# Kernel tuning notes

Measured on AMD Instinct MI355X. Metric: run time of the kernel, lower is better.

Reference implementation:

```python
import jax, jax.numpy as jnp
import numpy as np

N_NODES = 100000
N_EDGES = 1_600_000
N_ROIS = 400
HIDDEN = 128
N_GRAPHS = 512
OUT = 2


def setup_inputs() -> dict:
    key = jax.random.key(0)
    ks = jax.random.split(key, 7)
    x = jax.random.normal(ks[0], (N_NODES, N_ROIS), dtype=jnp.float32)
    edge_index = jax.random.randint(ks[1], (2, N_EDGES), 0, N_NODES, dtype=jnp.int32)
    # sorted graph-assignment vector; prepend arange so every graph id is non-empty
    rnd = jax.random.randint(ks[2], (N_NODES - N_GRAPHS,), 0, N_GRAPHS, dtype=jnp.int32)
    batch = jnp.sort(jnp.concatenate([jnp.arange(N_GRAPHS, dtype=jnp.int32), rnd]))
    W = jax.random.normal(ks[3], (N_ROIS, HIDDEN), dtype=jnp.float32) / np.float32(np.sqrt(N_ROIS))
    b = jnp.zeros((HIDDEN,), dtype=jnp.float32)
    lin_W = jax.random.normal(ks[4], (HIDDEN, OUT), dtype=jnp.float32) / np.float32(np.sqrt(HIDDEN))
    lin_b = jnp.zeros((OUT,), dtype=jnp.float32)
    return {"x": x, "edge_index": edge_index, "batch": batch,
            "W": W, "b": b, "lin_W": lin_W, "lin_b": lin_b}


def reference(x, edge_index, batch, W, b, lin_W, lin_b):
    N = x.shape[0]
    # GCNConv: add self-loops, symmetric normalization D^-1/2 (A+I) D^-1/2
    loops = jnp.arange(N, dtype=edge_index.dtype)
    row = jnp.concatenate([edge_index[0], loops])  # source
    col = jnp.concatenate([edge_index[1], loops])  # target
    deg = jax.ops.segment_sum(jnp.ones_like(col, dtype=x.dtype), col, num_segments=N)
    dinv = jnp.where(deg > 0, jax.lax.rsqrt(deg), 0.0)
    norm = dinv[row] * dinv[col]                   # [E+N]
    h = x @ W                                      # [N, H] transform before propagate
    msg = h[row] * norm[:, None]                   # [E+N, H]
    agg = jax.ops.segment_sum(msg, col, num_segments=N) + b
    act = jax.nn.relu(agg)                         # [N, H]
    # global max pool over graph ids (all segments guaranteed non-empty)
    pooled = jax.ops.segment_max(act, batch, num_segments=N_GRAPHS)  # [G, H]
    logits = pooled @ lin_W + lin_b                # [G, OUT]
    return logits, pooled
```

## Files before the change

kernel.cpp:

```cpp
#include <hip/hip_runtime.h>
#include <hip/hip_bf16.h>

#define N_NODES 100000
#define N_EDGES 1600000
#define N_ROIS  400
#define HID     128
#define N_GRAPHS 512
#define NOUT    2
#define NBUCK   391
#define BCAP    8192
#define ECH     4096
#define NPW     16
#define NBLK_BUCKET 391
#define NBLK_PREP   208
#define NBLK_GEMM   782

typedef __attribute__((ext_vector_type(8))) short short8;
typedef __attribute__((ext_vector_type(4))) float f32x4;

static __device__ __forceinline__ unsigned short f2bf(float f) {
  unsigned u = __float_as_uint(f);
  u += 0x7fffu + ((u >> 16) & 1u);
  return (unsigned short)(u >> 16);
}
static __device__ __forceinline__ float bf2f(unsigned short h) {
  return __uint_as_float(((unsigned)h) << 16);
}

static __device__ __forceinline__ void gload_lds16(const unsigned short* g, short* l) {
  __builtin_amdgcn_global_load_lds(
      (const __attribute__((address_space(1))) void*)g,
      (__attribute__((address_space(3))) void*)l, 16, 0, 0);
}

__global__ __launch_bounds__(256) void prep_bucket_k(
    const int* __restrict__ row, const int* __restrict__ col,
    int* __restrict__ bcnt, unsigned int* __restrict__ pairs,
    const float* __restrict__ W, unsigned short* __restrict__ Wf) {
  __shared__ int hist[NBUCK];
  __shared__ int base[NBUCK];
  int t = threadIdx.x;
  if (blockIdx.x >= NBLK_BUCKET) {
    int idx = (blockIdx.x - NBLK_BUCKET) * 256 + t;
    if (idx < 13 * 8 * 64 * 8) {
      int u    = idx & 7;
      int lane = (idx >> 3) & 63;
      int nt   = (idx >> 9) & 7;
      int kk5  = idx >> 12;
      int n = nt * 16 + (lane & 15);
      int k = kk5 * 32 + (lane >> 4) * 8 + u;
      Wf[idx] = (k < N_ROIS) ? f2bf(W[k * HID + n]) : (unsigned short)0;
    }
    return;
  }
  for (int b = t; b < NBUCK; b += 256) hist[b] = 0;
  __syncthreads();
  int e0 = blockIdx.x * ECH;
  unsigned int pk[16];
  int bk[16], rk[16];
#pragma unroll
  for (int i = 0; i < 16; ++i) {
    int e = e0 + t + i * 256;
    if (e < N_EDGES) {
      int r = row[e], c = col[e];
      bk[i] = c >> 8;
      pk[i] = ((unsigned)r << 8) | (unsigned)(c & 255);
      rk[i] = atomicAdd(&hist[bk[i]], 1);
    } else bk[i] = -1;
  }
  __syncthreads();
  for (int b = t; b < NBUCK; b += 256)
    base[b] = (hist[b] > 0) ? atomicAdd(&bcnt[b], hist[b]) : 0;
  __syncthreads();
#pragma unroll
  for (int i = 0; i < 16; ++i)
    if (bk[i] >= 0) {
      int p = base[bk[i]] + rk[i];
      if (p < BCAP) pairs[(size_t)bk[i] * BCAP + p] = pk[i];
    }
}

__global__ __launch_bounds__(512, 4) void csr_gemm_k(
    const unsigned int* __restrict__ pairs, const int* __restrict__ bcnt,
    int* __restrict__ csr_row, int* __restrict__ offs, int* __restrict__ cnt,
    float* __restrict__ dinv,
    const float* __restrict__ x, const unsigned short* __restrict__ Wf,
    unsigned short* __restrict__ hp) {
  __shared__ __align__(16) union {
    struct { unsigned int ep[BCAP]; int h[256]; int sc[256]; int cur[256]; } c;
    short Bs[28672];
  } u;
  int t = threadIdx.x;

  if (blockIdx.x < NBUCK) {
    bool act = t < 256;
    int b = blockIdx.x;
    int m = min(bcnt[b], BCAP);
    size_t base = (size_t)b * BCAP;
    for (int j = t; j < m; j += 512) u.c.ep[j] = pairs[base + j];
    if (act) u.c.h[t] = 0;
    __syncthreads();
    for (int j = t; j < m; j += 512) atomicAdd(&u.c.h[u.c.ep[j] & 255u], 1);
    __syncthreads();
    int myc = act ? u.c.h[t] : 0;
    int mycp = (myc + 3) & ~3;
    if (act) u.c.sc[t] = mycp;
    __syncthreads();
    for (int off = 1; off < 256; off <<= 1) {
      int v = (act && t >= off) ? u.c.sc[t - off] : 0;
      __syncthreads();
      if (act) u.c.sc[t] += v;
      __syncthreads();
    }
    if (act) {
      int loff = u.c.sc[t] - mycp;
      u.c.cur[t] = loff;
      int node = b * 256 + t;
      if (node < N_NODES) {
        cnt[node] = myc;
        offs[node] = (int)base + loff;
        dinv[node] = rsqrtf((float)(myc + 1));
      }
    }
    __syncthreads();
    for (int j = t; j < m; j += 512) {
      unsigned int e = u.c.ep[j];
      int pos = atomicAdd(&u.c.cur[e & 255u], 1);
      if (pos < BCAP) csr_row[base + pos] = (int)(e >> 8);
    }
    return;
  }

  int lane = t & 63, wv = t >> 6;
  int mrow = lane & 15, kg = lane >> 4;
  int row0 = (blockIdx.x - NBUCK) * 128;
  int arow = row0 + wv * 16 + mrow;
  bool rowok = arow < N_NODES;
  const float* xp = x + (size_t)arow * N_ROIS;

  f32x4 acc[8];
#pragma unroll
  for (int i = 0; i < 8; ++i) acc[i] = (f32x4){0.f, 0.f, 0.f, 0.f};

#pragma unroll
  for (int c = 0; c < 7; ++c) {
    int ch = wv * 7 + c;
    gload_lds16(Wf + (size_t)ch * 512 + lane * 8, &u.Bs[ch * 512]);
  }
  asm volatile("s_waitcnt vmcnt(0)" ::: "memory");
  __syncthreads();

#pragma unroll
  for (int kf = 0; kf < 7; ++kf) {
    int k0 = kf * 32 + kg * 8;
    short8 a8;
    if (rowok && k0 + 8 <= N_ROIS) {
      float4 f0 = *(const float4*)(xp + k0);
      float4 f1 = *(const float4*)(xp + k0 + 4);
      a8[0] = (short)f2bf(f0.x); a8[1] = (short)f2bf(f0.y);
      a8[2] = (short)f2bf(f0.z); a8[3] = (short)f2bf(f0.w);
      a8[4] = (short)f2bf(f1.x); a8[5] = (short)f2bf(f1.y);
      a8[6] = (short)f2bf(f1.z); a8[7] = (short)f2bf(f1.w);
    } else {
#pragma unroll
      for (int v = 0; v < 8; ++v) {
        int k = k0 + v;
        float f = (rowok && k < N_ROIS) ? xp[k] : 0.f;
        a8[v] = (short)f2bf(f);
      }
    }
#pragma unroll
    for (int nt = 0; nt < 8; ++nt) {
      short8 bf = *(const short8*)&u.Bs[(kf * 8 + nt) * 512 + lane * 8];
      acc[nt] = __builtin_amdgcn_mfma_f32_16x16x32_bf16(a8, bf, acc[nt], 0, 0, 0);
    }
  }
  __syncthreads();

#pragma unroll
  for (int c = 0; c < 6; ++c) {
    int ch = wv * 6 + c;
    gload_lds16(Wf + (size_t)(56 + ch) * 512 + lane * 8, &u.Bs[ch * 512]);
  }
  asm volatile("s_waitcnt vmcnt(0)" ::: "memory");
  __syncthreads();

#pragma unroll
  for (int kf = 0; kf < 6; ++kf) {
    int k0 = (kf + 7) * 32 + kg * 8;
    short8 a8;
    if (rowok && k0 + 8 <= N_ROIS) {
      float4 f0 = *(const float4*)(xp + k0);
      float4 f1 = *(const float4*)(xp + k0 + 4);
      a8[0] = (short)f2bf(f0.x); a8[1] = (short)f2bf(f0.y);
      a8[2] = (short)f2bf(f0.z); a8[3] = (short)f2bf(f0.w);
      a8[4] = (short)f2bf(f1.x); a8[5] = (short)f2bf(f1.y);
      a8[6] = (short)f2bf(f1.z); a8[7] = (short)f2bf(f1.w);
    } else {
#pragma unroll
      for (int v = 0; v < 8; ++v) {
        int k = k0 + v;
        float f = (rowok && k < N_ROIS) ? xp[k] : 0.f;
        a8[v] = (short)f2bf(f);
      }
    }
#pragma unroll
    for (int nt = 0; nt < 8; ++nt) {
      short8 bf = *(const short8*)&u.Bs[(kf * 8 + nt) * 512 + lane * 8];
      acc[nt] = __builtin_amdgcn_mfma_f32_16x16x32_bf16(a8, bf, acc[nt], 0, 0, 0);
    }
  }

#pragma unroll
  for (int r = 0; r < 4; ++r) {
    int grow = row0 + wv * 16 + kg * 4 + r;
    if (grow < N_NODES) {
      unsigned short* op = hp + (size_t)grow * HID + mrow;
#pragma unroll
      for (int nt = 0; nt < 8; ++nt) op[nt * 16] = f2bf(acc[nt][r]);
    }
  }
}

static __device__ __forceinline__ void acc8s(float* a, uint4 u, float d) {
  a[0] = fmaf(d, bf2f((unsigned short)(u.x)), a[0]);
  a[1] = fmaf(d, bf2f((unsigned short)(u.x >> 16)), a[1]);
  a[2] = fmaf(d, bf2f((unsigned short)(u.y)), a[2]);
  a[3] = fmaf(d, bf2f((unsigned short)(u.y >> 16)), a[3]);
  a[4] = fmaf(d, bf2f((unsigned short)(u.z)), a[4]);
  a[5] = fmaf(d, bf2f((unsigned short)(u.z >> 16)), a[5]);
  a[6] = fmaf(d, bf2f((unsigned short)(u.w)), a[6]);
  a[7] = fmaf(d, bf2f((unsigned short)(u.w >> 16)), a[7]);
}

__global__ __launch_bounds__(256) void gather_k(
    const unsigned short* __restrict__ hp, const int* __restrict__ csr_row,
    const int* __restrict__ offs, const int* __restrict__ cnt,
    const float* __restrict__ dinv, const int* __restrict__ batch,
    const float* __restrict__ bias, unsigned int* __restrict__ pooled_bits) {
  int wave = (blockIdx.x * blockDim.x + threadIdx.x) >> 6;
  int lane = threadIdx.x & 63;
  int g  = lane >> 4;
  int cg = lane & 15;
  int n0 = wave * NPW;
  if (n0 >= N_NODES) return;
  int nend = min(n0 + NPW, N_NODES);
  float bv[8];
  {
    float4 b0 = *(const float4*)(bias + cg * 8);
    float4 b1 = *(const float4*)(bias + cg * 8 + 4);
    bv[0] = b0.x; bv[1] = b0.y; bv[2] = b0.z; bv[3] = b0.w;
    bv[4] = b1.x; bv[5] = b1.y; bv[6] = b1.z; bv[7] = b1.w;
  }
  float rm[8];
#pragma unroll
  for (int k = 0; k < 8; ++k) rm[k] = 0.f;
  int cur_g = batch[n0];

  for (int i = n0; i < nend; ++i) {
    int start = offs[i];
    int m = cnt[i];
    float di = dinv[i];
    float a[8];
#pragma unroll
    for (int k = 0; k < 8; ++k) a[k] = 0.f;
    if (g == 0) {
      uint4 u = *(const uint4*)(hp + (size_t)i * HID + cg * 8);
      acc8s(a, u, di);
    }
    for (int j = 0; j < m; j += 4) {
      int4 q = *(const int4*)(csr_row + start + j);
      int s = (g == 0) ? q.x : (g == 1) ? q.y : (g == 2) ? q.z : q.w;
      if (j + g < m) {
        float dv = dinv[s];
        uint4 u = *(const uint4*)(hp + (size_t)s * HID + cg * 8);
        acc8s(a, u, dv);
      }
    }
#pragma unroll
    for (int k = 0; k < 8; ++k) {
      a[k] += __shfl_xor(a[k], 16);
      a[k] += __shfl_xor(a[k], 32);
    }
    int gb = batch[i];
    if (gb != cur_g) {
      if (lane < 16) {
#pragma unroll
        for (int k = 0; k < 8; ++k)
          atomicMax(&pooled_bits[cur_g * HID + cg * 8 + k], __float_as_uint(rm[k]));
      }
#pragma unroll
      for (int k = 0; k < 8; ++k) rm[k] = 0.f;
      cur_g = gb;
    }
#pragma unroll
    for (int k = 0; k < 8; ++k)
      rm[k] = fmaxf(rm[k], fmaxf(fmaf(di, a[k], bv[k]), 0.f));
  }
  if (lane < 16) {
#pragma unroll
    for (int k = 0; k < 8; ++k)
      atomicMax(&pooled_bits[cur_g * HID + cg * 8 + k], __float_as_uint(rm[k]));
  }
}

__global__ void logits_k(const float* __restrict__ pooled, const float* __restrict__ lin_W,
                         const float* __restrict__ lin_b, float* __restrict__ out) {
  int t = blockIdx.x * blockDim.x + threadIdx.x;
  if (t < N_GRAPHS * NOUT) {
    int g = t >> 1, o = t & 1;
    float s = lin_b[o];
    const float* pg = pooled + g * HID;
#pragma unroll 8
    for (int k = 0; k < HID; ++k) s = fmaf(pg[k], lin_W[k * NOUT + o], s);
    out[t] = s;
  }
}

extern "C" void kernel_launch(void* const* d_in, const int* in_sizes, int n_in,
                              void* d_out, int out_size, void* d_ws, size_t ws_size,
                              hipStream_t stream) {
  (void)in_sizes; (void)n_in; (void)ws_size;
  const float* x     = (const float*)d_in[0];
  const int*   ei    = (const int*)d_in[1];
  const int*   row   = ei;
  const int*   col   = ei + N_EDGES;
  const int*   batch = (const int*)d_in[2];
  const float* W     = (const float*)d_in[3];
  const float* b     = (const float*)d_in[4];
  const float* lin_W = (const float*)d_in[5];
  const float* lin_b = (const float*)d_in[6];
  float* out = (float*)d_out;

  char* ws = (char*)d_ws;
  int*   bcnt    = (int*)(ws + 0);
  int*   offs    = (int*)(ws + 4096);
  int*   cnt     = (int*)(ws + 404096);
  float* dinv    = (float*)(ws + 804096);
  unsigned short* Wf = (unsigned short*)(ws + 1204096);
  int*   csr_row = (int*)(ws + 1310720);
  unsigned int* pairs = (unsigned int*)(ws + 14123008);
  unsigned short* hp  = (unsigned short*)(ws + 26935296);

  hipMemsetAsync(bcnt, 0, NBUCK * sizeof(int), stream);
  hipMemsetAsync(d_out, 0, (size_t)out_size * sizeof(float), stream);

  prep_bucket_k<<<NBLK_BUCKET + NBLK_PREP, 256, 0, stream>>>(row, col, bcnt, pairs, W, Wf);
  csr_gemm_k<<<NBUCK + NBLK_GEMM, 512, 0, stream>>>(
      pairs, bcnt, csr_row, offs, cnt, dinv, x, Wf, hp);
  {
    int waves = (N_NODES + NPW - 1) / NPW;
    int blocks = (waves * 64 + 255) / 256;
    gather_k<<<blocks, 256, 0, stream>>>(
        hp, csr_row, offs, cnt, dinv, batch, b,
        (unsigned int*)(out + N_GRAPHS * NOUT));
  }
  logits_k<<<(N_GRAPHS * NOUT + 255) / 256, 256, 0, stream>>>(
      out + N_GRAPHS * NOUT, lin_W, lin_b, out);
}
```

Before: 385.5 us.

## Split hidden features into eight column slabs for cache-local gather

Measured after the change: 633.4 us. 1.64x slower.

```diff
diff --git a/kernel.cpp b/kernel.cpp
--- a/kernel.cpp
+++ b/kernel.cpp
@@ -14,6 +14,7 @@
 #define NBLK_BUCKET 391
 #define NBLK_PREP   208
 #define NBLK_GEMM   782
+#define SLAB ((size_t)N_NODES * 16)
 
 typedef __attribute__((ext_vector_type(8))) short short8;
 typedef __attribute__((ext_vector_type(4))) float f32x4;
@@ -85,7 +86,7 @@
     int* __restrict__ csr_row, int* __restrict__ offs, int* __restrict__ cnt,
     float* __restrict__ dinv,
     const float* __restrict__ x, const unsigned short* __restrict__ Wf,
-    unsigned short* __restrict__ hp) {
+    unsigned short* __restrict__ hp2) {
   __shared__ __align__(16) union {
     struct { unsigned int ep[BCAP]; int h[256]; int sc[256]; int cur[256]; } c;
     short Bs[28672];
@@ -215,9 +216,9 @@
   for (int r = 0; r < 4; ++r) {
     int grow = row0 + wv * 16 + kg * 4 + r;
     if (grow < N_NODES) {
-      unsigned short* op = hp + (size_t)grow * HID + mrow;
-#pragma unroll
-      for (int nt = 0; nt < 8; ++nt) op[nt * 16] = f2bf(acc[nt][r]);
+#pragma unroll
+      for (int nt = 0; nt < 8; ++nt)
+        hp2[(size_t)nt * SLAB + (size_t)grow * 16 + mrow] = f2bf(acc[nt][r]);
     }
   }
 }
@@ -234,21 +235,24 @@
 }
 
 __global__ __launch_bounds__(256) void gather_k(
-    const unsigned short* __restrict__ hp, const int* __restrict__ csr_row,
+    const unsigned short* __restrict__ hp2, const int* __restrict__ csr_row,
     const int* __restrict__ offs, const int* __restrict__ cnt,
     const float* __restrict__ dinv, const int* __restrict__ batch,
     const float* __restrict__ bias, unsigned int* __restrict__ pooled_bits) {
-  int wave = (blockIdx.x * blockDim.x + threadIdx.x) >> 6;
+  int slice = blockIdx.x & 7;
+  int bslot = blockIdx.x >> 3;
   int lane = threadIdx.x & 63;
-  int g  = lane >> 4;
-  int cg = lane & 15;
-  int n0 = wave * NPW;
+  int wv = threadIdx.x >> 6;
+  int n0 = (bslot * 4 + wv) * NPW;
   if (n0 >= N_NODES) return;
   int nend = min(n0 + NPW, N_NODES);
+  int es = lane >> 1;
+  int ch = lane & 1;
+  const unsigned short* hs = hp2 + (size_t)slice * SLAB;
   float bv[8];
   {
-    float4 b0 = *(const float4*)(bias + cg * 8);
-    float4 b1 = *(const float4*)(bias + cg * 8 + 4);
+    float4 b0 = *(const float4*)(bias + slice * 16 + ch * 8);
+    float4 b1 = *(const float4*)(bias + slice * 16 + ch * 8 + 4);
     bv[0] = b0.x; bv[1] = b0.y; bv[2] = b0.z; bv[3] = b0.w;
     bv[4] = b1.x; bv[5] = b1.y; bv[6] = b1.z; bv[7] = b1.w;
   }
@@ -264,30 +268,34 @@
     float a[8];
 #pragma unroll
     for (int k = 0; k < 8; ++k) a[k] = 0.f;
-    if (g == 0) {
-      uint4 u = *(const uint4*)(hp + (size_t)i * HID + cg * 8);
+    if (es == 0) {
+      uint4 u = *(const uint4*)(hs + (size_t)i * 16 + ch * 8);
       acc8s(a, u, di);
     }
-    for (int j = 0; j < m; j += 4) {
-      int4 q = *(const int4*)(csr_row + start + j);
-      int s = (g == 0) ? q.x : (g == 1) ? q.y : (g == 2) ? q.z : q.w;
-      if (j + g < m) {
+    for (int j = 0; j < m; j += 32) {
+      int idx = j + es;
+      if (idx < m) {
+        int s = csr_row[start + idx];
         float dv = dinv[s];
-        uint4 u = *(const uint4*)(hp + (size_t)s * HID + cg * 8);
+        uint4 u = *(const uint4*)(hs + (size_t)s * 16 + ch * 8);
         acc8s(a, u, dv);
       }
     }
 #pragma unroll
     for (int k = 0; k < 8; ++k) {
+      a[k] += __shfl_xor(a[k], 2);
+      a[k] += __shfl_xor(a[k], 4);
+      a[k] += __shfl_xor(a[k], 8);
       a[k] += __shfl_xor(a[k], 16);
       a[k] += __shfl_xor(a[k], 32);
     }
     int gb = batch[i];
     if (gb != cur_g) {
-      if (lane < 16) {
+      if (lane < 2) {
 #pragma unroll
         for (int k = 0; k < 8; ++k)
-          atomicMax(&pooled_bits[cur_g * HID + cg * 8 + k], __float_as_uint(rm[k]));
+          atomicMax(&pooled_bits[cur_g * HID + slice * 16 + ch * 8 + k],
+                    __float_as_uint(rm[k]));
       }
 #pragma unroll
       for (int k = 0; k < 8; ++k) rm[k] = 0.f;
@@ -297,10 +305,11 @@
     for (int k = 0; k < 8; ++k)
       rm[k] = fmaxf(rm[k], fmaxf(fmaf(di, a[k], bv[k]), 0.f));
   }
-  if (lane < 16) {
+  if (lane < 2) {
 #pragma unroll
     for (int k = 0; k < 8; ++k)
-      atomicMax(&pooled_bits[cur_g * HID + cg * 8 + k], __float_as_uint(rm[k]));
+      atomicMax(&pooled_bits[cur_g * HID + slice * 16 + ch * 8 + k],
+                __float_as_uint(rm[k]));
   }
 }
 
@@ -340,19 +349,19 @@
   unsigned short* Wf = (unsigned short*)(ws + 1204096);
   int*   csr_row = (int*)(ws + 1310720);
   unsigned int* pairs = (unsigned int*)(ws + 14123008);
-  unsigned short* hp  = (unsigned short*)(ws + 26935296);
+  unsigned short* hp2 = (unsigned short*)(ws + 26935296);
 
   hipMemsetAsync(bcnt, 0, NBUCK * sizeof(int), stream);
   hipMemsetAsync(d_out, 0, (size_t)out_size * sizeof(float), stream);
 
   prep_bucket_k<<<NBLK_BUCKET + NBLK_PREP, 256, 0, stream>>>(row, col, bcnt, pairs, W, Wf);
   csr_gemm_k<<<NBUCK + NBLK_GEMM, 512, 0, stream>>>(
-      pairs, bcnt, csr_row, offs, cnt, dinv, x, Wf, hp);
+      pairs, bcnt, csr_row, offs, cnt, dinv, x, Wf, hp2);
   {
-    int waves = (N_NODES + NPW - 1) / NPW;
-    int blocks = (waves * 64 + 255) / 256;
-    gather_k<<<blocks, 256, 0, stream>>>(
-        hp, csr_row, offs, cnt, dinv, batch, b,
+    int waves_per_slice = (N_NODES + NPW - 1) / NPW;
+    int blocks_per_slice = (waves_per_slice + 3) / 4;
+    gather_k<<<8 * blocks_per_slice, 256, 0, stream>>>(
+        hp2, csr_row, offs, cnt, dinv, batch, b,
         (unsigned int*)(out + N_GRAPHS * NOUT));
   }
   logits_k<<<(N_GRAPHS * NOUT + 255) / 256, 256, 0, stream>>>(
```

## Stage bucket scatters in LDS to coalesce global writes of pairs and CSR rows

Applied to the files above, without the earlier changes.

Result: no change. 381.7 us (-1.0%).

```diff
diff --git a/kernel.cpp b/kernel.cpp
--- a/kernel.cpp
+++ b/kernel.cpp
@@ -38,7 +38,11 @@
     int* __restrict__ bcnt, unsigned int* __restrict__ pairs,
     const float* __restrict__ W, unsigned short* __restrict__ Wf) {
   __shared__ int hist[NBUCK];
-  __shared__ int base[NBUCK];
+  __shared__ int lbase[NBUCK];
+  __shared__ int adj[NBUCK];
+  __shared__ unsigned int spk[ECH];
+  __shared__ unsigned short sbk[ECH];
+  __shared__ int sc[256];
   int t = threadIdx.x;
   if (blockIdx.x >= NBLK_BUCKET) {
     int idx = (blockIdx.x - NBLK_BUCKET) * 256 + t;
@@ -56,6 +60,7 @@
   for (int b = t; b < NBUCK; b += 256) hist[b] = 0;
   __syncthreads();
   int e0 = blockIdx.x * ECH;
+  int mtot = min(ECH, N_EDGES - e0);
   unsigned int pk[16];
   int bk[16], rk[16];
 #pragma unroll
@@ -69,15 +74,44 @@
     } else bk[i] = -1;
   }
   __syncthreads();
-  for (int b = t; b < NBUCK; b += 256)
-    base[b] = (hist[b] > 0) ? atomicAdd(&bcnt[b], hist[b]) : 0;
+  int v0 = hist[t];
+  sc[t] = v0;
+  __syncthreads();
+  for (int off = 1; off < 256; off <<= 1) {
+    int v = (t >= off) ? sc[t - off] : 0;
+    __syncthreads();
+    sc[t] += v;
+    __syncthreads();
+  }
+  lbase[t] = sc[t] - v0;
+  int tot0 = sc[255];
+  __syncthreads();
+  int v1 = (t < NBUCK - 256) ? hist[256 + t] : 0;
+  sc[t] = v1;
+  __syncthreads();
+  for (int off = 1; off < 256; off <<= 1) {
+    int v = (t >= off) ? sc[t - off] : 0;
+    __syncthreads();
+    sc[t] += v;
+    __syncthreads();
+  }
+  if (t < NBUCK - 256) lbase[256 + t] = tot0 + sc[t] - v1;
   __syncthreads();
 #pragma unroll
   for (int i = 0; i < 16; ++i)
     if (bk[i] >= 0) {
-      int p = base[bk[i]] + rk[i];
-      if (p < BCAP) pairs[(size_t)bk[i] * BCAP + p] = pk[i];
-    }
+      int pos = lbase[bk[i]] + rk[i];
+      spk[pos] = pk[i];
+      sbk[pos] = (unsigned short)bk[i];
+    }
+  for (int b = t; b < NBUCK; b += 256)
+    adj[b] = (hist[b] > 0) ? atomicAdd(&bcnt[b], hist[b]) : 0;
+  __syncthreads();
+  for (int j = t; j < mtot; j += 256) {
+    int b = sbk[j];
+    int p = adj[b] + (j - lbase[b]);
+    if (p < BCAP) pairs[(size_t)b * BCAP + p] = spk[j];
+  }
 }
 
 __global__ __launch_bounds__(512, 4) void csr_gemm_k(
@@ -87,7 +121,11 @@
     const float* __restrict__ x, const unsigned short* __restrict__ Wf,
     unsigned short* __restrict__ hp) {
   __shared__ __align__(16) union {
-    struct { unsigned int ep[BCAP]; int h[256]; int sc[256]; int cur[256]; } c;
+    struct {
+      unsigned int ep[BCAP];
+      int ssr[BCAP];
+      int h[256]; int sc2[256]; int cur[256];
+    } c;
     short Bs[28672];
   } u;
   int t = threadIdx.x;
@@ -104,16 +142,16 @@
     __syncthreads();
     int myc = act ? u.c.h[t] : 0;
     int mycp = (myc + 3) & ~3;
-    if (act) u.c.sc[t] = mycp;
+    if (act) u.c.sc2[t] = mycp;
     __syncthreads();
     for (int off = 1; off < 256; off <<= 1) {
-      int v = (act && t >= off) ? u.c.sc[t - off] : 0;
+      int v = (act && t >= off) ? u.c.sc2[t - off] : 0;
       __syncthreads();
-      if (act) u.c.sc[t] += v;
+      if (act) u.c.sc2[t] += v;
       __syncthreads();
     }
     if (act) {
-      int loff = u.c.sc[t] - mycp;
+      int loff = u.c.sc2[t] - mycp;
       u.c.cur[t] = loff;
       int node = b * 256 + t;
       if (node < N_NODES) {
@@ -126,8 +164,12 @@
     for (int j = t; j < m; j += 512) {
       unsigned int e = u.c.ep[j];
       int pos = atomicAdd(&u.c.cur[e & 255u], 1);
-      if (pos < BCAP) csr_row[base + pos] = (int)(e >> 8);
-    }
+      if (pos < BCAP) u.c.ssr[pos] = (int)(e >> 8);
+    }
+    __syncthreads();
+    int tpad = u.c.sc2[255];
+    if (tpad > BCAP) tpad = BCAP;
+    for (int j = t; j < tpad; j += 512) csr_row[base + j] = u.c.ssr[j];
     return;
   }
 
```
